# Performance work log

Hardware: AMD Instinct MI355X
Metric: run time of the kernel (lower is better)

Reference implementation:

```python
import jax, jax.numpy as jnp
import numpy as np

B, C, D, T = 8, 512, 256, 2048
EPS = 1e-5


def setup_inputs() -> dict:
    key = jax.random.key(0)
    ks = jax.random.split(key, 9)
    s_c = 1.0 / np.sqrt(C)
    s_d = 1.0 / np.sqrt(D)
    return {
        "inpt": jax.random.normal(ks[0], (B, C, T), dtype=jnp.float32),
        "theta_w": jax.random.uniform(ks[1], (D, C), jnp.float32, -s_c, s_c),
        "theta_b": jax.random.uniform(ks[2], (D,), jnp.float32, -s_c, s_c),
        "phi_w": jax.random.uniform(ks[3], (D, C), jnp.float32, -s_c, s_c),
        "phi_b": jax.random.uniform(ks[4], (D,), jnp.float32, -s_c, s_c),
        "g_w": jax.random.uniform(ks[5], (D, C), jnp.float32, -s_c, s_c),
        "g_b": jax.random.uniform(ks[6], (D,), jnp.float32, -s_c, s_c),
        "ht_w": jax.random.uniform(ks[7], (C, D), jnp.float32, -s_d, s_d),
        "ht_b": jax.random.uniform(ks[8], (C,), jnp.float32, -s_d, s_d),
        "bn_gamma": jnp.ones((C,), dtype=jnp.float32),
        "bn_beta": jnp.zeros((C,), dtype=jnp.float32),
    }


def reference(inpt, theta_w, theta_b, phi_w, phi_b, g_w, g_b, ht_w, ht_b, bn_gamma, bn_beta):
    # 1x1 convs are just channel-mixing matmuls: (B,C,T) -> (B,D,T)
    theta = jnp.einsum('dc,bct->bdt', theta_w, inpt) + theta_b[None, :, None]
    phi = jnp.einsum('dc,bct->bdt', phi_w, inpt) + phi_b[None, :, None]
    g = jnp.einsum('dc,bct->bdt', g_w, inpt) + g_b[None, :, None]
    # w[b,t,s] = sum_d theta[b,d,t] * phi[b,d,s]; softmax over s (phi time)
    w = jnp.einsum('bdt,bds->bts', theta, phi)
    w = jax.nn.softmax(w, axis=-1)
    # torch.matmul(g, w): out[b,d,s] = sum_t g[b,d,t] * w[b,t,s]
    attn = jnp.einsum('bdt,bts->bds', g, w)
    # ht 1x1 conv back to C channels
    h = jnp.einsum('cd,bdt->bct', ht_w, attn) + ht_b[None, :, None]
    # BatchNorm1d in training mode: batch stats over (B, T) per channel
    mean = jnp.mean(h, axis=(0, 2), keepdims=True)
    var = jnp.var(h, axis=(0, 2), keepdims=True)  # biased variance
    h_norm = (h - mean) * jax.lax.rsqrt(var + EPS)
    bn = bn_gamma[None, :, None] * h_norm + bn_beta[None, :, None]
    return inpt + bn
```

## Files before the change

kernel.cpp:

```cpp
#include <hip/hip_runtime.h>
#include <hip/hip_bf16.h>
#include <math.h>

#define Bx 8
#define Cx 512
#define Dx 256
#define Tx 2048
#define EPSx 1e-5f

typedef _Float16 h16;
typedef __attribute__((ext_vector_type(8))) _Float16 h16x8;
typedef __attribute__((ext_vector_type(8))) short s16x8;
typedef __attribute__((ext_vector_type(4))) float f32x4;

typedef __attribute__((address_space(3))) unsigned int lds_u32;
typedef __attribute__((address_space(1))) const unsigned int glb_u32;

__device__ __forceinline__ void cp16(void* ldsp, const void* g) {
    __builtin_amdgcn_global_load_lds((glb_u32*)g, (lds_u32*)ldsp, 16, 0, 0);
}

template<int MODE, bool BF>
__global__ __launch_bounds__(256, 4)
void gemm_mf(const h16* __restrict__ A, long aBatch, int lda,
             const h16* __restrict__ B, long bBatch, int ldb,
             void* __restrict__ C, long cBatch, int ldc,
             float* __restrict__ Cp, float* __restrict__ Z,
             int M, int N, int K, int mBlk,
             const float* __restrict__ biasM, const float* __restrict__ biasN) {
    __shared__ h16 As[128 * 64];
    __shared__ h16 Bs[128 * 64];
    const int tid  = threadIdx.x;
    const int lane = tid & 63, wid = tid >> 6;
    const int wm = (wid & 1) * 64, wn = (wid >> 1) * 64;
    const int lm = lane & 15, quad = lane >> 4;
    const unsigned id = blockIdx.x;
    const int b = id & 7;
    const unsigned rr = id >> 3;
    const int m0 = (rr % (unsigned)mBlk) * 128;
    const int n0 = (rr / (unsigned)mBlk) * 128;
    const h16* Ab = A + (size_t)b * aBatch + (size_t)m0 * lda;
    const h16* Bb = B + (size_t)b * bBatch + (size_t)n0 * ldb;

    const int srow  = tid >> 3;
    const int sclog = (tid & 7) ^ (srow & 7);
    char* ldsA = (char*)As + (tid & ~63) * 16;
    char* ldsB = (char*)Bs + (tid & ~63) * 16;

    f32x4 acc[4][4] = {};

    for (int k0 = 0; k0 < K; k0 += 64) {
        __syncthreads();
#pragma unroll
        for (int i = 0; i < 4; i++) {
            int r = srow + 32 * i;
            cp16(ldsA + i * 4096, Ab + (size_t)r * lda + k0 + sclog * 8);
        }
#pragma unroll
        for (int i = 0; i < 4; i++) {
            int r = srow + 32 * i;
            cp16(ldsB + i * 4096, Bb + (size_t)r * ldb + k0 + sclog * 8);
        }
        __syncthreads();
#pragma unroll
        for (int ks = 0; ks < 2; ks++) {
            s16x8 af[4], bf4[4];
#pragma unroll
            for (int i = 0; i < 4; i++) {
                int row = wm + 16 * i + lm;
                int st = (ks * 4 + quad) ^ (lm & 7);
                af[i] = *(const s16x8*)(As + row * 64 + st * 8);
            }
#pragma unroll
            for (int j = 0; j < 4; j++) {
                int row = wn + 16 * j + lm;
                int st = (ks * 4 + quad) ^ (lm & 7);
                bf4[j] = *(const s16x8*)(Bs + row * 64 + st * 8);
            }
#pragma unroll
            for (int i = 0; i < 4; i++)
#pragma unroll
                for (int j = 0; j < 4; j++) {
                    if constexpr (BF)
                        acc[i][j] = __builtin_amdgcn_mfma_f32_16x16x32_bf16(
                            af[i], bf4[j], acc[i][j], 0, 0, 0);
                    else
                        acc[i][j] = __builtin_amdgcn_mfma_f32_16x16x32_f16(
                            __builtin_bit_cast(h16x8, af[i]),
                            __builtin_bit_cast(h16x8, bf4[j]), acc[i][j], 0, 0, 0);
                }
        }
    }

    if constexpr (MODE == 0) {
        h16* Cb = (h16*)C + (size_t)b * cBatch;
#pragma unroll
        for (int i = 0; i < 4; i++)
#pragma unroll
            for (int j = 0; j < 4; j++) {
                int row = m0 + wm + 16 * i + quad * 4;
                int col = n0 + wn + 16 * j + lm;
                float bN = biasN ? biasN[col] : 0.0f;
#pragma unroll
                for (int r = 0; r < 4; r++) {
                    float v = acc[i][j][r] + bN;
                    if (biasM) v += biasM[row + r];
                    Cb[(size_t)(row + r) * ldc + col] = (h16)v;
                }
            }
    } else if constexpr (MODE == 1) {
        __hip_bfloat16* Cb = (__hip_bfloat16*)C + (size_t)b * cBatch;
#pragma unroll
        for (int j = 0; j < 4; j++) {
            int col = n0 + wn + 16 * j + lm;
            float iz = 1.0f / Z[(size_t)b * N + col];
#pragma unroll
            for (int i = 0; i < 4; i++) {
                int row = m0 + wm + 16 * i + quad * 4;
#pragma unroll
                for (int r = 0; r < 4; r++)
                    Cb[(size_t)(row + r) * ldc + col] =
                        __float2bfloat16(acc[i][j][r] * iz);
            }
        }
    } else if constexpr (MODE == 2) {
        __syncthreads();
        float* Zl = (float*)As;
        if (tid < 128) Zl[tid] = 0.0f;
        __syncthreads();
        __hip_bfloat16* Cb = (__hip_bfloat16*)C + (size_t)b * cBatch;
#pragma unroll
        for (int j = 0; j < 4; j++) {
            int cl = wn + 16 * j + lm;
            int col = n0 + cl;
            float zp = 0.0f;
#pragma unroll
            for (int i = 0; i < 4; i++) {
                int row = m0 + wm + 16 * i + quad * 4;
#pragma unroll
                for (int r = 0; r < 4; r++) {
                    float e = __expf(acc[i][j][r]);
                    zp += e;
                    Cb[(size_t)(row + r) * ldc + col] = __float2bfloat16(e);
                }
            }
            atomicAdd(&Zl[cl], zp);
        }
        __syncthreads();
        if (tid < 128) atomicAdd(&Z[(size_t)b * N + n0 + tid], Zl[tid]);
    } else {
        __syncthreads();
        float* Sl = (float*)As;
        float* Sq = Sl + 128;
        if (tid < 256) Sl[tid] = 0.0f;
        __syncthreads();
        h16* Cb = (h16*)C + (size_t)b * cBatch;
#pragma unroll
        for (int j = 0; j < 4; j++) {
            int cl = wn + 16 * j + lm;
            int col = n0 + cl;
            float bN = biasN[col];
            float s = 0.0f, q = 0.0f;
#pragma unroll
            for (int i = 0; i < 4; i++) {
                int row = m0 + wm + 16 * i + quad * 4;
#pragma unroll
                for (int r = 0; r < 4; r++) {
                    float v = acc[i][j][r] + bN;
                    s += v;
                    q = fmaf(v, v, q);
                    Cb[(size_t)(row + r) * ldc + col] = (h16)v;
                }
            }
            atomicAdd(&Sl[cl], s);
            atomicAdd(&Sq[cl], q);
        }
        __syncthreads();
        if (tid < 128) {
            atomicAdd(&Cp[n0 + tid], Sl[tid]);
            atomicAdd(&Z[n0 + tid], Sq[tid]);
        }
    }
}

__global__ __launch_bounds__(256)
void conv_x(const float* __restrict__ inpt, h16* __restrict__ xT) {
    __shared__ float lds[64][68];
    const int b = blockIdx.z;
    const int t0 = blockIdx.x * 64, c0 = blockIdx.y * 64;
    const int tid = threadIdx.x, q = tid >> 4, k = tid & 15;
    const float* ib = inpt + (size_t)b * Cx * Tx;
#pragma unroll
    for (int i = 0; i < 4; i++) {
        int c = q + 16 * i;
        float4 v = *(const float4*)(ib + (size_t)(c0 + c) * Tx + t0 + 4 * k);
        *(float4*)&lds[c][4 * k] = v;
    }
    __syncthreads();
    h16* xb = xT + (size_t)b * Tx * Cx;
#pragma unroll
    for (int i = 0; i < 4; i++) {
        int t = q + 16 * i;
        h16 o[4];
#pragma unroll
        for (int j = 0; j < 4; j++) o[j] = (h16)lds[4 * k + j][t];
        *(uint2*)(xb + (size_t)(t0 + t) * Cx + c0 + 4 * k) = *(uint2*)o;
    }
}

__global__ __launch_bounds__(256)
void conv_w(const float* __restrict__ w0, const float* __restrict__ w1,
            const float* __restrict__ w2, const float* __restrict__ w3,
            const float* __restrict__ tb, const float* __restrict__ pb,
            const float* __restrict__ gb,
            h16* __restrict__ dst, float* __restrict__ bias3,
            float* __restrict__ Z, float* __restrict__ psum,
            float* __restrict__ pssq) {
    int bx = blockIdx.x;
    int tid = threadIdx.x;
    if (bx == 577) {
        psum[tid] = 0.0f; psum[tid + 256] = 0.0f;
        pssq[tid] = 0.0f; pssq[tid + 256] = 0.0f;
        return;
    }
    if (bx >= 513) { Z[(bx - 513) * 256 + tid] = 0.0f; return; }
    if (bx == 512) {
        bias3[tid] = tb[tid];
        bias3[tid + 256] = pb[tid];
        bias3[tid + 512] = gb[tid];
        return;
    }
    int idx4 = bx * 256 + tid;
    int arr = idx4 >> 15, local4 = idx4 & 32767;
    const float* srcs[4] = {w0, w1, w2, w3};
    float4 v = ((const float4*)srcs[arr])[local4];
    h16 o[4] = {(h16)v.x, (h16)v.y, (h16)v.z, (h16)v.w};
    *(uint2*)(dst + (size_t)arr * 131072 + (size_t)local4 * 4) = *(uint2*)o;
}

__global__ __launch_bounds__(256)
void bn_apply_T(const float* __restrict__ inpt, const h16* __restrict__ hT,
                const float* __restrict__ psum, const float* __restrict__ pssq,
                const float* __restrict__ gamma, const float* __restrict__ beta,
                float* __restrict__ out) {
    __shared__ float lds[64][68];
    const int b = blockIdx.z, t0 = blockIdx.x * 64, c0 = blockIdx.y * 64;
    const int tid = threadIdx.x, q = tid >> 4, k = tid & 15;
    const h16* hb = hT + (size_t)b * Tx * Cx;
#pragma unroll
    for (int i = 0; i < 4; i++) {
        int t = q + 16 * i;
        uint2 raw = *(const uint2*)(hb + (size_t)(t0 + t) * Cx + c0 + 4 * k);
        const h16* hp = (const h16*)&raw;
        float4 v = make_float4((float)hp[0], (float)hp[1], (float)hp[2], (float)hp[3]);
        *(float4*)&lds[t][4 * k] = v;
    }
    __syncthreads();
    const float* ib = inpt + (size_t)b * Cx * Tx;
    float* ob = out + (size_t)b * Cx * Tx;
    const float invN = 1.0f / (float)(Bx * Tx);
#pragma unroll
    for (int i = 0; i < 4; i++) {
        int c = q + 16 * i;
        int cg = c0 + c;
        float mu = psum[cg] * invN;
        float var = pssq[cg] * invN - mu * mu;
        float rv = rsqrtf(var + EPSx);
        float ga = gamma[cg], be = beta[cg];
        float4 x = *(const float4*)(ib + (size_t)cg * Tx + t0 + 4 * k);
        float4 o;
        o.x = x.x + ga * (lds[4 * k + 0][c] - mu) * rv + be;
        o.y = x.y + ga * (lds[4 * k + 1][c] - mu) * rv + be;
        o.z = x.z + ga * (lds[4 * k + 2][c] - mu) * rv + be;
        o.w = x.w + ga * (lds[4 * k + 3][c] - mu) * rv + be;
        *(float4*)(ob + (size_t)cg * Tx + t0 + 4 * k) = o;
    }
}

extern "C" void kernel_launch(void* const* d_in, const int* in_sizes, int n_in,
                              void* d_out, int out_size, void* d_ws, size_t ws_size,
                              hipStream_t stream) {
    const float* inpt    = (const float*)d_in[0];
    const float* theta_w = (const float*)d_in[1];
    const float* theta_b = (const float*)d_in[2];
    const float* phi_w   = (const float*)d_in[3];
    const float* phi_b   = (const float*)d_in[4];
    const float* g_w     = (const float*)d_in[5];
    const float* g_b     = (const float*)d_in[6];
    const float* ht_w    = (const float*)d_in[7];
    const float* ht_b    = (const float*)d_in[8];
    const float* gamma   = (const float*)d_in[9];
    const float* beta    = (const float*)d_in[10];

    char* ws = (char*)d_ws;
    h16*   xT    = (h16*)(ws + 0);
    h16*   w4    = (h16*)(ws + 16777216);
    h16*   wHt   = w4 + 393216;
    float* bias3 = (float*)(ws + 17825792);
    float* Z     = (float*)(ws + 17828864);
    float* psum  = (float*)(ws + 17894400);
    float* pssq  = (float*)(ws + 17896448);
    h16*   thpg  = (h16*)(ws + 17902592);
    h16*   gh    = (h16*)(ws + 43068416);
    h16*   LT    = (h16*)(ws + 59845632);
    h16*   hT    = xT;

    const long sX  = (long)Tx * Cx;
    const long sTP = (long)Tx * 768;
    const long sGH = (long)Cx * Tx;
    const long sW  = (long)Tx * Tx;

    dim3 blk(256);
    conv_x<<<dim3(Tx / 64, Cx / 64, Bx), blk, 0, stream>>>(inpt, xT);
    conv_w<<<578, blk, 0, stream>>>(theta_w, phi_w, g_w, ht_w,
                                    theta_b, phi_b, g_b,
                                    w4, bias3, Z, psum, pssq);
    gemm_mf<0, false><<<dim3(768), blk, 0, stream>>>(
        xT, sX, Cx, w4, 0, Cx, thpg, sTP, 768, nullptr, nullptr,
        Tx, 768, Cx, 16, nullptr, bias3);
    gemm_mf<2, false><<<dim3(2048), blk, 0, stream>>>(
        thpg + 256, sTP, 768, thpg, sTP, 768, LT, sW, Tx, nullptr, Z,
        Tx, Tx, Dx, 16, nullptr, nullptr);
    gemm_mf<1, false><<<dim3(512), blk, 0, stream>>>(
        wHt, 0, Dx, thpg + 512, sTP, 768, gh, sGH, Tx, nullptr, Z,
        Cx, Tx, Dx, 4, nullptr, nullptr);
    gemm_mf<3, true><<<dim3(512), blk, 0, stream>>>(
        LT, sW, Tx, gh, sGH, Tx, hT, sX, Cx, psum, pssq,
        Tx, Cx, Tx, 16, nullptr, ht_b);
    bn_apply_T<<<dim3(Tx / 64, Cx / 64, Bx), blk, 0, stream>>>(
        inpt, hT, psum, pssq, gamma, beta, (float*)d_out);
}
```

Before: 225.7 us.

## Template GEMM N-tile width and fuse weight and input conversion kernels

Adds a TN template parameter to the MFMA GEMM so the final attention-times-values GEMM (K=2048) runs with 128x64 tiles and 1024 blocks instead of 512, giving more blocks across the CUs for that long-K kernel. The input-transpose and weight-conversion/zeroing kernels are merged into one launch, using an extra z-slice of blocks for the weight work, which removes one kernel launch. Smaller N tiles halve the B-operand reuse per block, so more A (LT) traffic is re-read from memory.

Result: no change. 224.1 us (-0.7%).

```diff
diff --git a/kernel.cpp b/kernel.cpp
--- a/kernel.cpp
+++ b/kernel.cpp
@@ -20,7 +20,7 @@
     __builtin_amdgcn_global_load_lds((glb_u32*)g, (lds_u32*)ldsp, 16, 0, 0);
 }
 
-template<int MODE, bool BF>
+template<int MODE, bool BF, int TN>
 __global__ __launch_bounds__(256, 4)
 void gemm_mf(const h16* __restrict__ A, long aBatch, int lda,
              const h16* __restrict__ B, long bBatch, int ldb,
@@ -28,17 +28,18 @@
              float* __restrict__ Cp, float* __restrict__ Z,
              int M, int N, int K, int mBlk,
              const float* __restrict__ biasM, const float* __restrict__ biasN) {
+    constexpr int NJ = TN / 32;
     __shared__ h16 As[128 * 64];
-    __shared__ h16 Bs[128 * 64];
+    __shared__ h16 Bs[TN * 64];
     const int tid  = threadIdx.x;
     const int lane = tid & 63, wid = tid >> 6;
-    const int wm = (wid & 1) * 64, wn = (wid >> 1) * 64;
+    const int wm = (wid & 1) * 64, wn = (wid >> 1) * (TN / 2);
     const int lm = lane & 15, quad = lane >> 4;
     const unsigned id = blockIdx.x;
     const int b = id & 7;
     const unsigned rr = id >> 3;
     const int m0 = (rr % (unsigned)mBlk) * 128;
-    const int n0 = (rr / (unsigned)mBlk) * 128;
+    const int n0 = (rr / (unsigned)mBlk) * TN;
     const h16* Ab = A + (size_t)b * aBatch + (size_t)m0 * lda;
     const h16* Bb = B + (size_t)b * bBatch + (size_t)n0 * ldb;
 
@@ -47,7 +48,7 @@
     char* ldsA = (char*)As + (tid & ~63) * 16;
     char* ldsB = (char*)Bs + (tid & ~63) * 16;
 
-    f32x4 acc[4][4] = {};
+    f32x4 acc[4][NJ] = {};
 
     for (int k0 = 0; k0 < K; k0 += 64) {
         __syncthreads();
@@ -57,14 +58,14 @@
             cp16(ldsA + i * 4096, Ab + (size_t)r * lda + k0 + sclog * 8);
         }
 #pragma unroll
-        for (int i = 0; i < 4; i++) {
+        for (int i = 0; i < TN / 32; i++) {
             int r = srow + 32 * i;
             cp16(ldsB + i * 4096, Bb + (size_t)r * ldb + k0 + sclog * 8);
         }
         __syncthreads();
 #pragma unroll
         for (int ks = 0; ks < 2; ks++) {
-            s16x8 af[4], bf4[4];
+            s16x8 af[4], bf4[NJ];
 #pragma unroll
             for (int i = 0; i < 4; i++) {
                 int row = wm + 16 * i + lm;
@@ -72,7 +73,7 @@
                 af[i] = *(const s16x8*)(As + row * 64 + st * 8);
             }
 #pragma unroll
-            for (int j = 0; j < 4; j++) {
+            for (int j = 0; j < NJ; j++) {
                 int row = wn + 16 * j + lm;
                 int st = (ks * 4 + quad) ^ (lm & 7);
                 bf4[j] = *(const s16x8*)(Bs + row * 64 + st * 8);
@@ -80,7 +81,7 @@
 #pragma unroll
             for (int i = 0; i < 4; i++)
 #pragma unroll
-                for (int j = 0; j < 4; j++) {
+                for (int j = 0; j < NJ; j++) {
                     if constexpr (BF)
                         acc[i][j] = __builtin_amdgcn_mfma_f32_16x16x32_bf16(
                             af[i], bf4[j], acc[i][j], 0, 0, 0);
@@ -97,7 +98,7 @@
 #pragma unroll
         for (int i = 0; i < 4; i++)
 #pragma unroll
-            for (int j = 0; j < 4; j++) {
+            for (int j = 0; j < NJ; j++) {
                 int row = m0 + wm + 16 * i + quad * 4;
                 int col = n0 + wn + 16 * j + lm;
                 float bN = biasN ? biasN[col] : 0.0f;
@@ -111,7 +112,7 @@
     } else if constexpr (MODE == 1) {
         __hip_bfloat16* Cb = (__hip_bfloat16*)C + (size_t)b * cBatch;
 #pragma unroll
-        for (int j = 0; j < 4; j++) {
+        for (int j = 0; j < NJ; j++) {
             int col = n0 + wn + 16 * j + lm;
             float iz = 1.0f / Z[(size_t)b * N + col];
 #pragma unroll
@@ -126,11 +127,11 @@
     } else if constexpr (MODE == 2) {
         __syncthreads();
         float* Zl = (float*)As;
-        if (tid < 128) Zl[tid] = 0.0f;
+        if (tid < TN) Zl[tid] = 0.0f;
         __syncthreads();
         __hip_bfloat16* Cb = (__hip_bfloat16*)C + (size_t)b * cBatch;
 #pragma unroll
-        for (int j = 0; j < 4; j++) {
+        for (int j = 0; j < NJ; j++) {
             int cl = wn + 16 * j + lm;
             int col = n0 + cl;
             float zp = 0.0f;
@@ -147,16 +148,16 @@
             atomicAdd(&Zl[cl], zp);
         }
         __syncthreads();
-        if (tid < 128) atomicAdd(&Z[(size_t)b * N + n0 + tid], Zl[tid]);
+        if (tid < TN) atomicAdd(&Z[(size_t)b * N + n0 + tid], Zl[tid]);
     } else {
         __syncthreads();
         float* Sl = (float*)As;
-        float* Sq = Sl + 128;
-        if (tid < 256) Sl[tid] = 0.0f;
+        float* Sq = Sl + TN;
+        if (tid < 2 * TN) Sl[tid] = 0.0f;
         __syncthreads();
         h16* Cb = (h16*)C + (size_t)b * cBatch;
 #pragma unroll
-        for (int j = 0; j < 4; j++) {
+        for (int j = 0; j < NJ; j++) {
             int cl = wn + 16 * j + lm;
             int col = n0 + cl;
             float bN = biasN[col];
@@ -176,7 +177,7 @@
             atomicAdd(&Sq[cl], q);
         }
         __syncthreads();
-        if (tid < 128) {
+        if (tid < TN) {
             atomicAdd(&Cp[n0 + tid], Sl[tid]);
             atomicAdd(&Z[n0 + tid], Sq[tid]);
         }
@@ -184,11 +185,40 @@
 }
 
 __global__ __launch_bounds__(256)
-void conv_x(const float* __restrict__ inpt, h16* __restrict__ xT) {
+void conv_prep(const float* __restrict__ inpt, h16* __restrict__ xT,
+               const float* __restrict__ w0, const float* __restrict__ w1,
+               const float* __restrict__ w2, const float* __restrict__ w3,
+               const float* __restrict__ tb, const float* __restrict__ pb,
+               const float* __restrict__ gb,
+               h16* __restrict__ dst, float* __restrict__ bias3,
+               float* __restrict__ Z, float* __restrict__ psum,
+               float* __restrict__ pssq) {
+    const int tid = threadIdx.x;
+    if (blockIdx.z == 8) {
+        int bx = blockIdx.y * 32 + blockIdx.x;
+#pragma unroll
+        for (int rep = 0; rep < 2; rep++) {
+            int idx4 = bx * 512 + rep * 256 + tid;
+            int arr = idx4 >> 15, local4 = idx4 & 32767;
+            const float* srcs[4] = {w0, w1, w2, w3};
+            float4 v = ((const float4*)srcs[arr])[local4];
+            h16 o[4] = {(h16)v.x, (h16)v.y, (h16)v.z, (h16)v.w};
+            *(uint2*)(dst + (size_t)arr * 131072 + (size_t)local4 * 4) = *(uint2*)o;
+        }
+        if (bx < 64) Z[bx * 256 + tid] = 0.0f;
+        if (bx == 64) bias3[tid] = tb[tid];
+        if (bx == 65) bias3[256 + tid] = pb[tid];
+        if (bx == 66) bias3[512 + tid] = gb[tid];
+        if (bx == 67) {
+            psum[tid] = 0.0f; psum[tid + 256] = 0.0f;
+            pssq[tid] = 0.0f; pssq[tid + 256] = 0.0f;
+        }
+        return;
+    }
     __shared__ float lds[64][68];
     const int b = blockIdx.z;
     const int t0 = blockIdx.x * 64, c0 = blockIdx.y * 64;
-    const int tid = threadIdx.x, q = tid >> 4, k = tid & 15;
+    const int q = tid >> 4, k = tid & 15;
     const float* ib = inpt + (size_t)b * Cx * Tx;
 #pragma unroll
     for (int i = 0; i < 4; i++) {
@@ -206,36 +236,6 @@
         for (int j = 0; j < 4; j++) o[j] = (h16)lds[4 * k + j][t];
         *(uint2*)(xb + (size_t)(t0 + t) * Cx + c0 + 4 * k) = *(uint2*)o;
     }
-}
-
-__global__ __launch_bounds__(256)
-void conv_w(const float* __restrict__ w0, const float* __restrict__ w1,
-            const float* __restrict__ w2, const float* __restrict__ w3,
-            const float* __restrict__ tb, const float* __restrict__ pb,
-            const float* __restrict__ gb,
-            h16* __restrict__ dst, float* __restrict__ bias3,
-            float* __restrict__ Z, float* __restrict__ psum,
-            float* __restrict__ pssq) {
-    int bx = blockIdx.x;
-    int tid = threadIdx.x;
-    if (bx == 577) {
-        psum[tid] = 0.0f; psum[tid + 256] = 0.0f;
-        pssq[tid] = 0.0f; pssq[tid + 256] = 0.0f;
-        return;
-    }
-    if (bx >= 513) { Z[(bx - 513) * 256 + tid] = 0.0f; return; }
-    if (bx == 512) {
-        bias3[tid] = tb[tid];
-        bias3[tid + 256] = pb[tid];
-        bias3[tid + 512] = gb[tid];
-        return;
-    }
-    int idx4 = bx * 256 + tid;
-    int arr = idx4 >> 15, local4 = idx4 & 32767;
-    const float* srcs[4] = {w0, w1, w2, w3};
-    float4 v = ((const float4*)srcs[arr])[local4];
-    h16 o[4] = {(h16)v.x, (h16)v.y, (h16)v.z, (h16)v.w};
-    *(uint2*)(dst + (size_t)arr * 131072 + (size_t)local4 * 4) = *(uint2*)o;
 }
 
 __global__ __launch_bounds__(256)
@@ -311,20 +311,19 @@
     const long sW  = (long)Tx * Tx;
 
     dim3 blk(256);
-    conv_x<<<dim3(Tx / 64, Cx / 64, Bx), blk, 0, stream>>>(inpt, xT);
-    conv_w<<<578, blk, 0, stream>>>(theta_w, phi_w, g_w, ht_w,
-                                    theta_b, phi_b, g_b,
-                                    w4, bias3, Z, psum, pssq);
-    gemm_mf<0, false><<<dim3(768), blk, 0, stream>>>(
+    conv_prep<<<dim3(Tx / 64, Cx / 64, Bx + 1), blk, 0, stream>>>(
+        inpt, xT, theta_w, phi_w, g_w, ht_w, theta_b, phi_b, g_b,
+        w4, bias3, Z, psum, pssq);
+    gemm_mf<0, false, 128><<<dim3(768), blk, 0, stream>>>(
         xT, sX, Cx, w4, 0, Cx, thpg, sTP, 768, nullptr, nullptr,
         Tx, 768, Cx, 16, nullptr, bias3);
-    gemm_mf<2, false><<<dim3(2048), blk, 0, stream>>>(
+    gemm_mf<2, false, 128><<<dim3(2048), blk, 0, stream>>>(
         thpg + 256, sTP, 768, thpg, sTP, 768, LT, sW, Tx, nullptr, Z,
         Tx, Tx, Dx, 16, nullptr, nullptr);
-    gemm_mf<1, false><<<dim3(512), blk, 0, stream>>>(
+    gemm_mf<1, false, 128><<<dim3(512), blk, 0, stream>>>(
         wHt, 0, Dx, thpg + 512, sTP, 768, gh, sGH, Tx, nullptr, Z,
         Cx, Tx, Dx, 4, nullptr, nullptr);
-    gemm_mf<3, true><<<dim3(512), blk, 0, stream>>>(
+    gemm_mf<3, true, 64><<<dim3(1024), blk, 0, stream>>>(
         LT, sW, Tx, gh, sGH, Tx, hT, sX, Cx, psum, pssq,
         Tx, Cx, Tx, 16, nullptr, ht_b);
     bn_apply_T<<<dim3(Tx / 64, Cx / 64, Bx), blk, 0, stream>>>(
```
